# Performance work log

Measured on AMD Instinct MI355X. Metric: run time of the kernel, lower is better.

## Reference

```python
import jax, jax.numpy as jnp
import numpy as np

HEADS = 8
EPS = 1e-4

def pixel_norm(x):
    # faithful to source: mean over dim=1 (token axis for [B,T,C] tensors)
    return x / jnp.sqrt(jnp.mean(x * x, axis=1, keepdims=True) + EPS)

def setup_inputs() -> dict:
    key = jax.random.key(0)
    ks = jax.random.split(key, 6)
    B, T, C = 4, 2048, 512
    s = 1.0 / np.sqrt(C)
    return {
        "hidden_states": jax.random.normal(ks[0], (B, T, C), jnp.float32),
        "Wq": jax.random.normal(ks[1], (C, C), jnp.float32) * s,
        "Wk": jax.random.normal(ks[2], (C, C), jnp.float32) * s,
        "Wv": jax.random.normal(ks[3], (C, C), jnp.float32) * s,
        "Wo": jax.random.normal(ks[4], (C, C), jnp.float32) * s,
        "bo": jnp.zeros((C,), jnp.float32),
    }

def reference(hidden_states, Wq, Wk, Wv, Wo, bo):
    B, T, C = hidden_states.shape
    H = HEADS
    d = C // H
    scale = 1.0 / np.sqrt(d)  # attn.scale = head_dim**-0.5
    residual = hidden_states

    q = pixel_norm(hidden_states @ Wq)  # [B,T,C]
    k = pixel_norm(hidden_states @ Wk)
    v = pixel_norm(hidden_states @ Wv)

    # head_to_batch_dim: [B,T,C] -> [B,H,T,d]
    def split_heads(x):
        return x.reshape(B, T, H, d).transpose(0, 2, 1, 3)
    q, k, v = split_heads(q), split_heads(k), split_heads(v)

    scores = jnp.einsum("bhqd,bhkd->bhqk", q, k) * scale
    probs = jax.nn.softmax(scores, axis=-1)
    out = jnp.einsum("bhqk,bhkd->bhqd", probs, v)  # [B,H,T,d]

    # batch_to_head_dim: [B,H,T,d] -> [B,T,C]
    out = out.transpose(0, 2, 1, 3).reshape(B, T, C)
    out = out @ Wo + bo  # to_out[0]; to_out[1] is dropout (identity in eval)
    out = out + residual  # residual_connection
    return out  # rescale_output_factor = 1.0
```

## Files before the change

kernel.cpp:

```cpp
#include <hip/hip_runtime.h>

#define Tt 2048
#define Cc 512
#define Bb 4
#define BC (Bb * Cc)

typedef __attribute__((ext_vector_type(4))) float f32x4;
typedef __attribute__((ext_vector_type(8))) _Float16 f16x8;
typedef __attribute__((ext_vector_type(4))) _Float16 f16x4;
typedef __attribute__((ext_vector_type(2))) _Float16 f16x2;

__device__ static inline void gl16(const _Float16* g, _Float16* l)
{
    __builtin_amdgcn_global_load_lds(
        (const __attribute__((address_space(1))) void*)g,
        (__attribute__((address_space(3))) void*)l, 16, 0, 0);
}

__global__ __launch_bounds__(256) void wsetup(
    const float* __restrict__ Wq, const float* __restrict__ Wk,
    const float* __restrict__ Wv, const float* __restrict__ Wo,
    _Float16* __restrict__ Wt)
{
    const int z = blockIdx.y;
    const float* W = (z == 0) ? Wq : (z == 1) ? Wk : (z == 2) ? Wv : Wo;
    const int k0 = (blockIdx.x >> 3) * 64, n0 = (blockIdx.x & 7) * 64;
    const int tid = threadIdx.x;
    __shared__ float tile[64][65];

#pragma unroll
    for (int i = 0; i < 4; ++i) {
        const int idx = i * 256 + tid;
        const int kr = idx >> 4, c4 = idx & 15;
        float4 v = *(const float4*)&W[(size_t)(k0 + kr) * Cc + n0 + c4 * 4];
        tile[kr][c4 * 4 + 0] = v.x; tile[kr][c4 * 4 + 1] = v.y;
        tile[kr][c4 * 4 + 2] = v.z; tile[kr][c4 * 4 + 3] = v.w;
    }
    __syncthreads();
#pragma unroll
    for (int i = 0; i < 4; ++i) {
        const int idx = i * 256 + tid;
        const int nr = idx >> 4, k4 = idx & 15;
        f16x4 o;
        o[0] = (_Float16)tile[k4 * 4 + 0][nr];
        o[1] = (_Float16)tile[k4 * 4 + 1][nr];
        o[2] = (_Float16)tile[k4 * 4 + 2][nr];
        o[3] = (_Float16)tile[k4 * 4 + 3][nr];
        *(f16x4*)&Wt[((size_t)(z * 512 + n0 + nr)) * Cc + k0 + k4 * 4] = o;
    }
}

__global__ __launch_bounds__(256) void hs_half(
    const float* __restrict__ HS, _Float16* __restrict__ HSh)
{
    const size_t i = ((size_t)blockIdx.x * 256 + threadIdx.x) * 8;
    float4 a = *(const float4*)&HS[i];
    float4 b = *(const float4*)&HS[i + 4];
    f16x8 o;
    o[0] = (_Float16)a.x; o[1] = (_Float16)a.y;
    o[2] = (_Float16)a.z; o[3] = (_Float16)a.w;
    o[4] = (_Float16)b.x; o[5] = (_Float16)b.y;
    o[6] = (_Float16)b.z; o[7] = (_Float16)b.w;
    *(f16x8*)&HSh[i] = o;
}

__global__ __launch_bounds__(256, 3) void qkv_mfma(
    const _Float16* __restrict__ HSh, const _Float16* __restrict__ Wt,
    _Float16* __restrict__ Qf, _Float16* __restrict__ Kf,
    _Float16* __restrict__ Vf, float* __restrict__ colsum)
{
    const int mt = blockIdx.x;
    const int nt = blockIdx.y;
    const int z  = blockIdx.z;
    _Float16* Out = (z == 0) ? Qf : (z == 1) ? Kf : Vf;

    const int tid = threadIdx.x;
    const int wave = tid >> 6, lane = tid & 63;
    const int quad = lane >> 4, lm = lane & 15;
    const int wm = (wave & 1) * 64, wn = (wave >> 1) * 64;

    __shared__ _Float16 sA[128 * 32];
    __shared__ _Float16 sB[128 * 32];

    f32x4 acc[4][4];
#pragma unroll
    for (int mf = 0; mf < 4; ++mf)
#pragma unroll
        for (int nf = 0; nf < 4; ++nf) acc[mf][nf] = (f32x4){0.f, 0.f, 0.f, 0.f};

    const int lr = lane >> 2;
    const int lc = (lane & 3) * 8;
    const _Float16* gaA = HSh + (size_t)(mt * 128 + wave * 32 + lr) * Cc + lc;
    const _Float16* gaB = Wt + ((size_t)(z * 512 + nt * 128 + wave * 32 + lr)) * Cc + lc;
    _Float16* ldA = &sA[wave * 1024];
    _Float16* ldB = &sB[wave * 1024];

    for (int k0 = 0; k0 < Cc; k0 += 32) {
        __syncthreads();
        gl16(gaA + k0,            ldA);
        gl16(gaA + 16 * Cc + k0,  ldA + 512);
        gl16(gaB + k0,            ldB);
        gl16(gaB + 16 * Cc + k0,  ldB + 512);
        __syncthreads();

        f16x8 ah[4], bh[4];
#pragma unroll
        for (int mf = 0; mf < 4; ++mf)
            ah[mf] = *(const f16x8*)&sA[(wm + mf * 16 + lm) * 32 + quad * 8];
#pragma unroll
        for (int nf = 0; nf < 4; ++nf)
            bh[nf] = *(const f16x8*)&sB[(wn + nf * 16 + lm) * 32 + quad * 8];
#pragma unroll
        for (int mf = 0; mf < 4; ++mf)
#pragma unroll
            for (int nf = 0; nf < 4; ++nf)
                acc[mf][nf] = __builtin_amdgcn_mfma_f32_16x16x32_f16(ah[mf], bh[nf], acc[mf][nf], 0, 0, 0);
    }

    const int bidx = mt >> 4;
#pragma unroll
    for (int nf = 0; nf < 4; ++nf) {
        float cs = 0.f;
#pragma unroll
        for (int mf = 0; mf < 4; ++mf)
#pragma unroll
            for (int r = 0; r < 4; ++r) {
                const float v = acc[mf][nf][r];
                const size_t idx =
                    (size_t)(mt * 128 + wm + mf * 16 + quad * 4 + r) * Cc +
                    nt * 128 + wn + nf * 16 + lm;
                Out[idx] = (_Float16)v;
                cs += v * v;
            }
        cs += __shfl_xor(cs, 16, 64);
        cs += __shfl_xor(cs, 32, 64);
        if (lane < 16)
            atomicAdd(&colsum[(size_t)z * BC + bidx * Cc + nt * 128 + wn + nf * 16 + lane], cs);
    }
}

__global__ void inv_norm_kernel(const float* __restrict__ colsum,
                                float* __restrict__ inv)
{
    const int i = blockIdx.x * blockDim.x + threadIdx.x;
    if (i < 3 * BC) inv[i] = rsqrtf(colsum[i] * (1.0f / Tt) + 1e-4f);
}

__global__ __launch_bounds__(256) void norm_vt(
    const _Float16* __restrict__ V, _Float16* __restrict__ VT)
{
    const int blk = blockIdx.x;
    const int b = blk >> 8, ct = (blk >> 5) & 7, tt = blk & 31;
    const int t0 = tt * 64, c0 = ct * 64;
    const int tid = threadIdx.x;

    __shared__ _Float16 tile[64 * 72];

#pragma unroll
    for (int i = 0; i < 2; ++i) {
        const int idx = i * 256 + tid;
        const int tr = idx >> 3, c8 = (idx & 7) * 8;
        *(f16x8*)&tile[tr * 72 + c8] =
            *(const f16x8*)&V[(size_t)(b * Tt + t0 + tr) * Cc + c0 + c8];
    }
    __syncthreads();
#pragma unroll
    for (int i = 0; i < 2; ++i) {
        const int idx = i * 256 + tid;
        const int cr = idx >> 3, u = idx & 7;
        const int C0 = ((u >> 2) & 1) * 32 + (u & 1) * 16 + ((u >> 1) & 1) * 4;
        f16x4 oa, ob;
#pragma unroll
        for (int j = 0; j < 4; ++j) oa[j] = tile[(u * 8 + j) * 72 + cr];
#pragma unroll
        for (int j = 0; j < 4; ++j) ob[j] = tile[(u * 8 + 4 + j) * 72 + cr];
        _Float16* dst = &VT[(size_t)(b * Cc + c0 + cr) * Tt + t0];
        *(f16x4*)&dst[C0]     = oa;
        *(f16x4*)&dst[C0 + 8] = ob;
    }
}

#define LSTR 72

__global__ __launch_bounds__(256, 3) void attn_mfma(
    const _Float16* __restrict__ Qf, const _Float16* __restrict__ Kf,
    const _Float16* __restrict__ VT, const float* __restrict__ inv,
    _Float16* __restrict__ AO)
{
    const int bid = blockIdx.x;
    const int qt = bid >> 5;
    const int bh = bid & 31;
    const int b = bh >> 3, h = bh & 7;
    const int tid = threadIdx.x;
    const int wave = tid >> 6, lane = tid & 63;
    const int quad = lane >> 4, lm = lane & 15;

    __shared__ _Float16 sK[2][64 * LSTR];
    __shared__ _Float16 sVT[2][64 * LSTR];

    f16x8 qb[2][2];
    {
        const float* iqp = inv + b * Cc + h * 64;
        const float* ikp = inv + BC + b * Cc + h * 64;
#pragma unroll
        for (int qf = 0; qf < 2; ++qf) {
            const int row = qt * 128 + wave * 32 + qf * 16 + lm;
#pragma unroll
            for (int ks = 0; ks < 2; ++ks) {
                const int d0 = ks * 32 + quad * 8;
                f16x8 qv = *(const f16x8*)&Qf[(size_t)(b * Tt + row) * Cc + h * 64 + d0];
#pragma unroll
                for (int j = 0; j < 8; ++j) {
                    const float f = (float)qv[j] * iqp[d0 + j] * ikp[d0 + j] * 0.18033688011f;
                    qb[qf][ks][j] = (_Float16)f;
                }
            }
        }
    }

    f32x4 o[4][2];
#pragma unroll
    for (int cf = 0; cf < 4; ++cf)
#pragma unroll
        for (int qf = 0; qf < 2; ++qf) o[cf][qf] = (f32x4){0.f, 0.f, 0.f, 0.f};
    f32x4 ol[2];
#pragma unroll
    for (int qf = 0; qf < 2; ++qf) ol[qf] = (f32x4){0.f, 0.f, 0.f, 0.f};
    f16x8 ones;
#pragma unroll
    for (int j = 0; j < 8; ++j) ones[j] = (_Float16)1.0f;

    f16x8 pb[2][2];
#pragma unroll
    for (int qf = 0; qf < 2; ++qf)
#pragma unroll
        for (int ks = 0; ks < 2; ++ks)
#pragma unroll
            for (int j = 0; j < 8; ++j) pb[qf][ks][j] = (_Float16)0.0f;

    const int sr0 = tid >> 3, sc0 = (tid & 7) * 8;
    const int sr1 = sr0 + 32;
    const _Float16* gK = Kf + (size_t)b * Tt * Cc + h * 64;
    const _Float16* gV = VT + ((size_t)b * Cc + h * 64) * Tt;

    f16x8 rk0, rk1, rv0, rv1;
    {
        rk0 = *(const f16x8*)&gK[(size_t)sr0 * Cc + sc0];
        rk1 = *(const f16x8*)&gK[(size_t)sr1 * Cc + sc0];
        rv0 = *(const f16x8*)&gV[(size_t)sr0 * Tt + sc0];
        rv1 = *(const f16x8*)&gV[(size_t)sr1 * Tt + sc0];
    }

#pragma unroll 2
    for (int kt = 0; kt < 32; ++kt) {
        const int cur = kt & 1, prv = cur ^ 1;
        _Float16* sKc = sK[cur];
        _Float16* sVc = sVT[cur];

        __syncthreads();
        *(f16x8*)&sKc[sr0 * LSTR + sc0] = rk0;
        *(f16x8*)&sKc[sr1 * LSTR + sc0] = rk1;
        *(f16x8*)&sVc[sr0 * LSTR + sc0] = rv0;
        *(f16x8*)&sVc[sr1 * LSTR + sc0] = rv1;
        __syncthreads();

        if (kt < 31) {
            const int t0 = (kt + 1) * 64;
            rk0 = *(const f16x8*)&gK[(size_t)(t0 + sr0) * Cc + sc0];
            rk1 = *(const f16x8*)&gK[(size_t)(t0 + sr1) * Cc + sc0];
            rv0 = *(const f16x8*)&gV[(size_t)sr0 * Tt + t0 + sc0];
            rv1 = *(const f16x8*)&gV[(size_t)sr1 * Tt + t0 + sc0];
        }

        f32x4 st[4][2];
#pragma unroll
        for (int kf = 0; kf < 4; ++kf)
#pragma unroll
            for (int qf = 0; qf < 2; ++qf) st[kf][qf] = (f32x4){0.f, 0.f, 0.f, 0.f};
#pragma unroll
        for (int ks = 0; ks < 2; ++ks) {
            f16x8 ka[4];
#pragma unroll
            for (int kf = 0; kf < 4; ++kf)
                ka[kf] = *(const f16x8*)&sKc[(kf * 16 + lm) * LSTR + ks * 32 + quad * 8];
            __builtin_amdgcn_s_setprio(1);
#pragma unroll
            for (int kf = 0; kf < 4; ++kf)
#pragma unroll
                for (int qf = 0; qf < 2; ++qf)
                    st[kf][qf] = __builtin_amdgcn_mfma_f32_16x16x32_f16(ka[kf], qb[qf][ks], st[kf][qf], 0, 0, 0);
            __builtin_amdgcn_s_setprio(0);
        }

        if (kt > 0) {
            _Float16* sVp = sVT[prv];
#pragma unroll
            for (int ks = 0; ks < 2; ++ks) {
                f16x8 va[4];
#pragma unroll
                for (int cf = 0; cf < 4; ++cf)
                    va[cf] = *(const f16x8*)&sVp[(cf * 16 + lm) * LSTR + ks * 32 + quad * 8];
                __builtin_amdgcn_s_setprio(1);
#pragma unroll
                for (int cf = 0; cf < 4; ++cf)
#pragma unroll
                    for (int qf = 0; qf < 2; ++qf)
                        o[cf][qf] = __builtin_amdgcn_mfma_f32_16x16x32_f16(va[cf], pb[qf][ks], o[cf][qf], 0, 0, 0);
#pragma unroll
                for (int qf = 0; qf < 2; ++qf)
                    ol[qf] = __builtin_amdgcn_mfma_f32_16x16x32_f16(ones, pb[qf][ks], ol[qf], 0, 0, 0);
                __builtin_amdgcn_s_setprio(0);
            }
        }

#pragma unroll
        for (int ks = 0; ks < 2; ++ks)
#pragma unroll
            for (int qf = 0; qf < 2; ++qf) {
                const f32x4 a = st[2 * ks][qf];
                const f32x4 c = st[2 * ks + 1][qf];
                const f16x2 l0 = __builtin_bit_cast(f16x2, __builtin_amdgcn_cvt_pkrtz(
                    __builtin_amdgcn_exp2f(a[0]), __builtin_amdgcn_exp2f(a[1])));
                const f16x2 l1 = __builtin_bit_cast(f16x2, __builtin_amdgcn_cvt_pkrtz(
                    __builtin_amdgcn_exp2f(a[2]), __builtin_amdgcn_exp2f(a[3])));
                const f16x2 h0 = __builtin_bit_cast(f16x2, __builtin_amdgcn_cvt_pkrtz(
                    __builtin_amdgcn_exp2f(c[0]), __builtin_amdgcn_exp2f(c[1])));
                const f16x2 h1 = __builtin_bit_cast(f16x2, __builtin_amdgcn_cvt_pkrtz(
                    __builtin_amdgcn_exp2f(c[2]), __builtin_amdgcn_exp2f(c[3])));
                f16x8 p;
                p[0] = l0[0]; p[1] = l0[1]; p[2] = l1[0]; p[3] = l1[1];
                p[4] = h0[0]; p[5] = h0[1]; p[6] = h1[0]; p[7] = h1[1];
                pb[qf][ks] = p;
            }
    }

    {
        _Float16* sVp = sVT[1];
#pragma unroll
        for (int ks = 0; ks < 2; ++ks) {
            f16x8 va[4];
#pragma unroll
            for (int cf = 0; cf < 4; ++cf)
                va[cf] = *(const f16x8*)&sVp[(cf * 16 + lm) * LSTR + ks * 32 + quad * 8];
#pragma unroll
            for (int cf = 0; cf < 4; ++cf)
#pragma unroll
                for (int qf = 0; qf < 2; ++qf)
                    o[cf][qf] = __builtin_amdgcn_mfma_f32_16x16x32_f16(va[cf], pb[qf][ks], o[cf][qf], 0, 0, 0);
#pragma unroll
            for (int qf = 0; qf < 2; ++qf)
                ol[qf] = __builtin_amdgcn_mfma_f32_16x16x32_f16(ones, pb[qf][ks], ol[qf], 0, 0, 0);
        }
    }

    float il[2];
#pragma unroll
    for (int qf = 0; qf < 2; ++qf) il[qf] = 1.0f / ol[qf][0];
    const float* ivp = inv + 2 * BC + b * Cc + h * 64;
    float iv[4][4];
#pragma unroll
    for (int cf = 0; cf < 4; ++cf) {
        float4 t = *(const float4*)&ivp[cf * 16 + quad * 4];
        iv[cf][0] = t.x; iv[cf][1] = t.y; iv[cf][2] = t.z; iv[cf][3] = t.w;
    }
#pragma unroll
    for (int qf = 0; qf < 2; ++qf) {
        const size_t row = (size_t)(b * Tt + qt * 128 + wave * 32 + qf * 16 + lm);
#pragma unroll
        for (int cf = 0; cf < 4; ++cf) {
            f16x4 pk;
#pragma unroll
            for (int r = 0; r < 4; ++r)
                pk[r] = (_Float16)(o[cf][qf][r] * il[qf] * iv[cf][r]);
            *(f16x4*)&AO[row * Cc + h * 64 + cf * 16 + quad * 4] = pk;
        }
    }
}

__global__ __launch_bounds__(256, 2) void out_mfma(
    const _Float16* __restrict__ AO, const _Float16* __restrict__ Wt,
    const float* __restrict__ bo, const float* __restrict__ HS,
    float* __restrict__ Outp)
{
    const int mt = blockIdx.x;
    const int nt = blockIdx.y;
    const int tid = threadIdx.x;
    const int wave = tid >> 6, lane = tid & 63;
    const int quad = lane >> 4, lm = lane & 15;
    const int wm = (wave & 1) * 32, wn = (wave >> 1) * 64;

    __shared__ _Float16 sA[64 * 32];
    __shared__ _Float16 sB[128 * 32];

    f32x4 acc[2][4];
#pragma unroll
    for (int mf = 0; mf < 2; ++mf)
#pragma unroll
        for (int nf = 0; nf < 4; ++nf) acc[mf][nf] = (f32x4){0.f, 0.f, 0.f, 0.f};

    const int lr = lane >> 2;
    const int lc = (lane & 3) * 8;
    const _Float16* gaA = AO + (size_t)(mt * 64 + wave * 16 + lr) * Cc + lc;
    const _Float16* gaB = Wt + ((size_t)(3 * 512 + nt * 128 + wave * 32 + lr)) * Cc + lc;
    _Float16* ldA = &sA[wave * 512];
    _Float16* ldB = &sB[wave * 1024];

    for (int k0 = 0; k0 < Cc; k0 += 32) {
        __syncthreads();
        gl16(gaA + k0,           ldA);
        gl16(gaB + k0,           ldB);
        gl16(gaB + 16 * Cc + k0, ldB + 512);
        __syncthreads();

        f16x8 ah[2], bh[4];
#pragma unroll
        for (int mf = 0; mf < 2; ++mf)
            ah[mf] = *(const f16x8*)&sA[(wm + mf * 16 + lm) * 32 + quad * 8];
#pragma unroll
        for (int nf = 0; nf < 4; ++nf)
            bh[nf] = *(const f16x8*)&sB[(wn + nf * 16 + lm) * 32 + quad * 8];
#pragma unroll
        for (int mf = 0; mf < 2; ++mf)
#pragma unroll
            for (int nf = 0; nf < 4; ++nf)
                acc[mf][nf] = __builtin_amdgcn_mfma_f32_16x16x32_f16(ah[mf], bh[nf], acc[mf][nf], 0, 0, 0);
    }

#pragma unroll
    for (int mf = 0; mf < 2; ++mf)
#pragma unroll
        for (int r = 0; r < 4; ++r) {
            const size_t m = (size_t)(mt * 64 + wm + mf * 16 + quad * 4 + r);
#pragma unroll
            for (int nf = 0; nf < 4; ++nf) {
                const int col = nt * 128 + wn + nf * 16 + lm;
                Outp[m * Cc + col] = acc[mf][nf][r] + bo[col] + HS[m * Cc + col];
            }
        }
}

extern "C" void kernel_launch(void* const* d_in, const int* in_sizes, int n_in,
                              void* d_out, int out_size, void* d_ws,
                              size_t ws_size, hipStream_t stream)
{
    const float* HS = (const float*)d_in[0];
    const float* Wq = (const float*)d_in[1];
    const float* Wk = (const float*)d_in[2];
    const float* Wv = (const float*)d_in[3];
    const float* Wo = (const float*)d_in[4];
    const float* bo = (const float*)d_in[5];
    float* out = (float*)d_out;

    const size_t SZ = (size_t)Bb * Tt * Cc;
    _Float16* Qf  = (_Float16*)d_ws;
    _Float16* Kf  = Qf + SZ;
    _Float16* Vf  = Kf + SZ;
    _Float16* VTh = Vf + SZ;
    _Float16* AO  = VTh + SZ;
    _Float16* Wt  = AO + SZ;
    float* colsum = (float*)(Wt + 4 * Cc * Cc);
    float* inv    = colsum + 3 * BC;

    _Float16* HSh = VTh;

    (void)hipMemsetAsync(colsum, 0, 3 * BC * sizeof(float), stream);

    wsetup<<<dim3(64, 4), 256, 0, stream>>>(Wq, Wk, Wv, Wo, Wt);

    hs_half<<<2048, 256, 0, stream>>>(HS, HSh);

    qkv_mfma<<<dim3(64, 4, 3), 256, 0, stream>>>(HSh, Wt, Qf, Kf, Vf, colsum);

    inv_norm_kernel<<<(3 * BC + 255) / 256, 256, 0, stream>>>(colsum, inv);

    norm_vt<<<1024, 256, 0, stream>>>(Vf, VTh);

    attn_mfma<<<dim3(512), 256, 0, stream>>>(Qf, Kf, VTh, inv, AO);

    out_mfma<<<dim3(128, 4), 256, 0, stream>>>(AO, Wt, bo, HS, out);
}
```

Baseline: 163.0 us.

## Merge prep launches and process 128-key blocks per barrier in attention

Weight transpose, hidden-state fp16 cast, and colsum zeroing move into a single prep kernel, and the inverse-norm computation is folded into the norm_vt launch as extra blocks. This removes a memset and two kernel launches. The attention loop now stages two 64-key K/V tiles per barrier pair, which halves the synchronisation count and keeps more loads in flight. In exchange it uses more LDS and registers, so the launch bound drops to 2 blocks per CU.

Measured after the change: 163.5 us. About the same (+0.3%).

```diff
diff --git a/kernel.cpp b/kernel.cpp
--- a/kernel.cpp
+++ b/kernel.cpp
@@ -17,51 +17,56 @@
         (__attribute__((address_space(3))) void*)l, 16, 0, 0);
 }
 
-__global__ __launch_bounds__(256) void wsetup(
+__global__ __launch_bounds__(256) void prep(
     const float* __restrict__ Wq, const float* __restrict__ Wk,
     const float* __restrict__ Wv, const float* __restrict__ Wo,
-    _Float16* __restrict__ Wt)
-{
-    const int z = blockIdx.y;
-    const float* W = (z == 0) ? Wq : (z == 1) ? Wk : (z == 2) ? Wv : Wo;
-    const int k0 = (blockIdx.x >> 3) * 64, n0 = (blockIdx.x & 7) * 64;
+    const float* __restrict__ HS, _Float16* __restrict__ Wt,
+    _Float16* __restrict__ HSh, float* __restrict__ colsum)
+{
+    const int blk = blockIdx.x;
     const int tid = threadIdx.x;
     __shared__ float tile[64][65];
 
-#pragma unroll
-    for (int i = 0; i < 4; ++i) {
-        const int idx = i * 256 + tid;
-        const int kr = idx >> 4, c4 = idx & 15;
-        float4 v = *(const float4*)&W[(size_t)(k0 + kr) * Cc + n0 + c4 * 4];
-        tile[kr][c4 * 4 + 0] = v.x; tile[kr][c4 * 4 + 1] = v.y;
-        tile[kr][c4 * 4 + 2] = v.z; tile[kr][c4 * 4 + 3] = v.w;
-    }
-    __syncthreads();
-#pragma unroll
-    for (int i = 0; i < 4; ++i) {
-        const int idx = i * 256 + tid;
-        const int nr = idx >> 4, k4 = idx & 15;
-        f16x4 o;
-        o[0] = (_Float16)tile[k4 * 4 + 0][nr];
-        o[1] = (_Float16)tile[k4 * 4 + 1][nr];
-        o[2] = (_Float16)tile[k4 * 4 + 2][nr];
-        o[3] = (_Float16)tile[k4 * 4 + 3][nr];
-        *(f16x4*)&Wt[((size_t)(z * 512 + n0 + nr)) * Cc + k0 + k4 * 4] = o;
-    }
-}
-
-__global__ __launch_bounds__(256) void hs_half(
-    const float* __restrict__ HS, _Float16* __restrict__ HSh)
-{
-    const size_t i = ((size_t)blockIdx.x * 256 + threadIdx.x) * 8;
-    float4 a = *(const float4*)&HS[i];
-    float4 b = *(const float4*)&HS[i + 4];
-    f16x8 o;
-    o[0] = (_Float16)a.x; o[1] = (_Float16)a.y;
-    o[2] = (_Float16)a.z; o[3] = (_Float16)a.w;
-    o[4] = (_Float16)b.x; o[5] = (_Float16)b.y;
-    o[6] = (_Float16)b.z; o[7] = (_Float16)b.w;
-    *(f16x8*)&HSh[i] = o;
+    if (blk < 2048) {
+        const size_t i = ((size_t)blk * 256 + tid) * 8;
+        float4 a = *(const float4*)&HS[i];
+        float4 b = *(const float4*)&HS[i + 4];
+        f16x8 o;
+        o[0] = (_Float16)a.x; o[1] = (_Float16)a.y;
+        o[2] = (_Float16)a.z; o[3] = (_Float16)a.w;
+        o[4] = (_Float16)b.x; o[5] = (_Float16)b.y;
+        o[6] = (_Float16)b.z; o[7] = (_Float16)b.w;
+        *(f16x8*)&HSh[i] = o;
+    } else if (blk < 2304) {
+        const int lb = blk - 2048;
+        const int z = lb >> 6, x = lb & 63;
+        const float* W = (z == 0) ? Wq : (z == 1) ? Wk : (z == 2) ? Wv : Wo;
+        const int k0 = (x >> 3) * 64, n0 = (x & 7) * 64;
+#pragma unroll
+        for (int i = 0; i < 4; ++i) {
+            const int idx = i * 256 + tid;
+            const int kr = idx >> 4, c4 = idx & 15;
+            float4 v = *(const float4*)&W[(size_t)(k0 + kr) * Cc + n0 + c4 * 4];
+            tile[kr][c4 * 4 + 0] = v.x; tile[kr][c4 * 4 + 1] = v.y;
+            tile[kr][c4 * 4 + 2] = v.z; tile[kr][c4 * 4 + 3] = v.w;
+        }
+        __syncthreads();
+#pragma unroll
+        for (int i = 0; i < 4; ++i) {
+            const int idx = i * 256 + tid;
+            const int nr = idx >> 4, k4 = idx & 15;
+            f16x4 o;
+            o[0] = (_Float16)tile[k4 * 4 + 0][nr];
+            o[1] = (_Float16)tile[k4 * 4 + 1][nr];
+            o[2] = (_Float16)tile[k4 * 4 + 2][nr];
+            o[3] = (_Float16)tile[k4 * 4 + 3][nr];
+            *(f16x4*)&Wt[((size_t)(z * 512 + n0 + nr)) * Cc + k0 + k4 * 4] = o;
+        }
+    } else {
+        const int i = (blk - 2304) * 2048 + tid * 8;
+        *(f32x4*)&colsum[i]     = (f32x4){0.f, 0.f, 0.f, 0.f};
+        *(f32x4*)&colsum[i + 4] = (f32x4){0.f, 0.f, 0.f, 0.f};
+    }
 }
 
 __global__ __launch_bounds__(256, 3) void qkv_mfma(
@@ -139,22 +144,23 @@
     }
 }
 
-__global__ void inv_norm_kernel(const float* __restrict__ colsum,
-                                float* __restrict__ inv)
-{
-    const int i = blockIdx.x * blockDim.x + threadIdx.x;
-    if (i < 3 * BC) inv[i] = rsqrtf(colsum[i] * (1.0f / Tt) + 1e-4f);
-}
-
 __global__ __launch_bounds__(256) void norm_vt(
-    const _Float16* __restrict__ V, _Float16* __restrict__ VT)
+    const _Float16* __restrict__ V, _Float16* __restrict__ VT,
+    const float* __restrict__ colsum, float* __restrict__ inv)
 {
     const int blk = blockIdx.x;
+    const int tid = threadIdx.x;
+
+    __shared__ _Float16 tile[64 * 72];
+
+    if (blk >= 1024) {
+        const int i = (blk - 1024) * 256 + tid;
+        inv[i] = rsqrtf(colsum[i] * (1.0f / Tt) + 1e-4f);
+        return;
+    }
+
     const int b = blk >> 8, ct = (blk >> 5) & 7, tt = blk & 31;
     const int t0 = tt * 64, c0 = ct * 64;
-    const int tid = threadIdx.x;
-
-    __shared__ _Float16 tile[64 * 72];
 
 #pragma unroll
     for (int i = 0; i < 2; ++i) {
@@ -182,7 +188,7 @@
 
 #define LSTR 72
 
-__global__ __launch_bounds__(256, 3) void attn_mfma(
+__global__ __launch_bounds__(256, 2) void attn_mfma(
     const _Float16* __restrict__ Qf, const _Float16* __restrict__ Kf,
     const _Float16* __restrict__ VT, const float* __restrict__ inv,
     _Float16* __restrict__ AO)
@@ -196,7 +202,7 @@
     const int quad = lane >> 4, lm = lane & 15;
 
     __shared__ _Float16 sK[2][64 * LSTR];
-    __shared__ _Float16 sVT[2][64 * LSTR];
+    __shared__ _Float16 sVT[2][2][64 * LSTR];
 
     f16x8 qb[2][2];
     {
@@ -243,99 +249,113 @@
     const _Float16* gK = Kf + (size_t)b * Tt * Cc + h * 64;
     const _Float16* gV = VT + ((size_t)b * Cc + h * 64) * Tt;
 
-    f16x8 rk0, rk1, rv0, rv1;
+    f16x8 rka0, rka1, rva0, rva1;
+    f16x8 rkb0, rkb1, rvb0, rvb1;
     {
-        rk0 = *(const f16x8*)&gK[(size_t)sr0 * Cc + sc0];
-        rk1 = *(const f16x8*)&gK[(size_t)sr1 * Cc + sc0];
-        rv0 = *(const f16x8*)&gV[(size_t)sr0 * Tt + sc0];
-        rv1 = *(const f16x8*)&gV[(size_t)sr1 * Tt + sc0];
+        rka0 = *(const f16x8*)&gK[(size_t)sr0 * Cc + sc0];
+        rka1 = *(const f16x8*)&gK[(size_t)sr1 * Cc + sc0];
+        rva0 = *(const f16x8*)&gV[(size_t)sr0 * Tt + sc0];
+        rva1 = *(const f16x8*)&gV[(size_t)sr1 * Tt + sc0];
+        rkb0 = *(const f16x8*)&gK[(size_t)(64 + sr0) * Cc + sc0];
+        rkb1 = *(const f16x8*)&gK[(size_t)(64 + sr1) * Cc + sc0];
+        rvb0 = *(const f16x8*)&gV[(size_t)sr0 * Tt + 64 + sc0];
+        rvb1 = *(const f16x8*)&gV[(size_t)sr1 * Tt + 64 + sc0];
     }
 
 #pragma unroll 2
-    for (int kt = 0; kt < 32; ++kt) {
-        const int cur = kt & 1, prv = cur ^ 1;
-        _Float16* sKc = sK[cur];
-        _Float16* sVc = sVT[cur];
-
-        __syncthreads();
-        *(f16x8*)&sKc[sr0 * LSTR + sc0] = rk0;
-        *(f16x8*)&sKc[sr1 * LSTR + sc0] = rk1;
-        *(f16x8*)&sVc[sr0 * LSTR + sc0] = rv0;
-        *(f16x8*)&sVc[sr1 * LSTR + sc0] = rv1;
-        __syncthreads();
-
-        if (kt < 31) {
-            const int t0 = (kt + 1) * 64;
-            rk0 = *(const f16x8*)&gK[(size_t)(t0 + sr0) * Cc + sc0];
-            rk1 = *(const f16x8*)&gK[(size_t)(t0 + sr1) * Cc + sc0];
-            rv0 = *(const f16x8*)&gV[(size_t)sr0 * Tt + t0 + sc0];
-            rv1 = *(const f16x8*)&gV[(size_t)sr1 * Tt + t0 + sc0];
-        }
-
-        f32x4 st[4][2];
-#pragma unroll
-        for (int kf = 0; kf < 4; ++kf)
-#pragma unroll
-            for (int qf = 0; qf < 2; ++qf) st[kf][qf] = (f32x4){0.f, 0.f, 0.f, 0.f};
-#pragma unroll
-        for (int ks = 0; ks < 2; ++ks) {
-            f16x8 ka[4];
+    for (int r = 0; r < 16; ++r) {
+        const int g = r & 1;
+
+        __syncthreads();
+        *(f16x8*)&sK[0][sr0 * LSTR + sc0] = rka0;
+        *(f16x8*)&sK[0][sr1 * LSTR + sc0] = rka1;
+        *(f16x8*)&sVT[g][0][sr0 * LSTR + sc0] = rva0;
+        *(f16x8*)&sVT[g][0][sr1 * LSTR + sc0] = rva1;
+        *(f16x8*)&sK[1][sr0 * LSTR + sc0] = rkb0;
+        *(f16x8*)&sK[1][sr1 * LSTR + sc0] = rkb1;
+        *(f16x8*)&sVT[g][1][sr0 * LSTR + sc0] = rvb0;
+        *(f16x8*)&sVT[g][1][sr1 * LSTR + sc0] = rvb1;
+        __syncthreads();
+
+        if (r < 15) {
+            const int tn = (r + 1) * 128;
+            rka0 = *(const f16x8*)&gK[(size_t)(tn + sr0) * Cc + sc0];
+            rka1 = *(const f16x8*)&gK[(size_t)(tn + sr1) * Cc + sc0];
+            rva0 = *(const f16x8*)&gV[(size_t)sr0 * Tt + tn + sc0];
+            rva1 = *(const f16x8*)&gV[(size_t)sr1 * Tt + tn + sc0];
+            rkb0 = *(const f16x8*)&gK[(size_t)(tn + 64 + sr0) * Cc + sc0];
+            rkb1 = *(const f16x8*)&gK[(size_t)(tn + 64 + sr1) * Cc + sc0];
+            rvb0 = *(const f16x8*)&gV[(size_t)sr0 * Tt + tn + 64 + sc0];
+            rvb1 = *(const f16x8*)&gV[(size_t)sr1 * Tt + tn + 64 + sc0];
+        }
+
+#pragma unroll
+        for (int half = 0; half < 2; ++half) {
+            f32x4 st[4][2];
 #pragma unroll
             for (int kf = 0; kf < 4; ++kf)
-                ka[kf] = *(const f16x8*)&sKc[(kf * 16 + lm) * LSTR + ks * 32 + quad * 8];
-            __builtin_amdgcn_s_setprio(1);
-#pragma unroll
-            for (int kf = 0; kf < 4; ++kf)
-#pragma unroll
-                for (int qf = 0; qf < 2; ++qf)
-                    st[kf][qf] = __builtin_amdgcn_mfma_f32_16x16x32_f16(ka[kf], qb[qf][ks], st[kf][qf], 0, 0, 0);
-            __builtin_amdgcn_s_setprio(0);
-        }
-
-        if (kt > 0) {
-            _Float16* sVp = sVT[prv];
+#pragma unroll
+                for (int qf = 0; qf < 2; ++qf) st[kf][qf] = (f32x4){0.f, 0.f, 0.f, 0.f};
 #pragma unroll
             for (int ks = 0; ks < 2; ++ks) {
-                f16x8 va[4];
-#pragma unroll
-                for (int cf = 0; cf < 4; ++cf)
-                    va[cf] = *(const f16x8*)&sVp[(cf * 16 + lm) * LSTR + ks * 32 + quad * 8];
+                f16x8 ka[4];
+#pragma unroll
+                for (int kf = 0; kf < 4; ++kf)
+                    ka[kf] = *(const f16x8*)&sK[half][(kf * 16 + lm) * LSTR + ks * 32 + quad * 8];
                 __builtin_amdgcn_s_setprio(1);
 #pragma unroll
-                for (int cf = 0; cf < 4; ++cf)
+                for (int kf = 0; kf < 4; ++kf)
 #pragma unroll
                     for (int qf = 0; qf < 2; ++qf)
-                        o[cf][qf] = __builtin_amdgcn_mfma_f32_16x16x32_f16(va[cf], pb[qf][ks], o[cf][qf], 0, 0, 0);
-#pragma unroll
-                for (int qf = 0; qf < 2; ++qf)
-                    ol[qf] = __builtin_amdgcn_mfma_f32_16x16x32_f16(ones, pb[qf][ks], ol[qf], 0, 0, 0);
+                        st[kf][qf] = __builtin_amdgcn_mfma_f32_16x16x32_f16(ka[kf], qb[qf][ks], st[kf][qf], 0, 0, 0);
                 __builtin_amdgcn_s_setprio(0);
             }
-        }
-
-#pragma unroll
-        for (int ks = 0; ks < 2; ++ks)
-#pragma unroll
-            for (int qf = 0; qf < 2; ++qf) {
-                const f32x4 a = st[2 * ks][qf];
-                const f32x4 c = st[2 * ks + 1][qf];
-                const f16x2 l0 = __builtin_bit_cast(f16x2, __builtin_amdgcn_cvt_pkrtz(
-                    __builtin_amdgcn_exp2f(a[0]), __builtin_amdgcn_exp2f(a[1])));
-                const f16x2 l1 = __builtin_bit_cast(f16x2, __builtin_amdgcn_cvt_pkrtz(
-                    __builtin_amdgcn_exp2f(a[2]), __builtin_amdgcn_exp2f(a[3])));
-                const f16x2 h0 = __builtin_bit_cast(f16x2, __builtin_amdgcn_cvt_pkrtz(
-                    __builtin_amdgcn_exp2f(c[0]), __builtin_amdgcn_exp2f(c[1])));
-                const f16x2 h1 = __builtin_bit_cast(f16x2, __builtin_amdgcn_cvt_pkrtz(
-                    __builtin_amdgcn_exp2f(c[2]), __builtin_amdgcn_exp2f(c[3])));
-                f16x8 p;
-                p[0] = l0[0]; p[1] = l0[1]; p[2] = l1[0]; p[3] = l1[1];
-                p[4] = h0[0]; p[5] = h0[1]; p[6] = h1[0]; p[7] = h1[1];
-                pb[qf][ks] = p;
+
+            if (half == 1 || r > 0) {
+                const _Float16* sVp = (half == 0) ? sVT[g ^ 1][1] : sVT[g][0];
+#pragma unroll
+                for (int ks = 0; ks < 2; ++ks) {
+                    f16x8 va[4];
+#pragma unroll
+                    for (int cf = 0; cf < 4; ++cf)
+                        va[cf] = *(const f16x8*)&sVp[(cf * 16 + lm) * LSTR + ks * 32 + quad * 8];
+                    __builtin_amdgcn_s_setprio(1);
+#pragma unroll
+                    for (int cf = 0; cf < 4; ++cf)
+#pragma unroll
+                        for (int qf = 0; qf < 2; ++qf)
+                            o[cf][qf] = __builtin_amdgcn_mfma_f32_16x16x32_f16(va[cf], pb[qf][ks], o[cf][qf], 0, 0, 0);
+#pragma unroll
+                    for (int qf = 0; qf < 2; ++qf)
+                        ol[qf] = __builtin_amdgcn_mfma_f32_16x16x32_f16(ones, pb[qf][ks], ol[qf], 0, 0, 0);
+                    __builtin_amdgcn_s_setprio(0);
+                }
             }
+
+#pragma unroll
+            for (int ks = 0; ks < 2; ++ks)
+#pragma unroll
+                for (int qf = 0; qf < 2; ++qf) {
+                    const f32x4 a = st[2 * ks][qf];
+                    const f32x4 c = st[2 * ks + 1][qf];
+                    const f16x2 l0 = __builtin_bit_cast(f16x2, __builtin_amdgcn_cvt_pkrtz(
+                        __builtin_amdgcn_exp2f(a[0]), __builtin_amdgcn_exp2f(a[1])));
+                    const f16x2 l1 = __builtin_bit_cast(f16x2, __builtin_amdgcn_cvt_pkrtz(
+                        __builtin_amdgcn_exp2f(a[2]), __builtin_amdgcn_exp2f(a[3])));
+                    const f16x2 h0 = __builtin_bit_cast(f16x2, __builtin_amdgcn_cvt_pkrtz(
+                        __builtin_amdgcn_exp2f(c[0]), __builtin_amdgcn_exp2f(c[1])));
+                    const f16x2 h1 = __builtin_bit_cast(f16x2, __builtin_amdgcn_cvt_pkrtz(
+                        __builtin_amdgcn_exp2f(c[2]), __builtin_amdgcn_exp2f(c[3])));
+                    f16x8 p;
+                    p[0] = l0[0]; p[1] = l0[1]; p[2] = l1[0]; p[3] = l1[1];
+                    p[4] = h0[0]; p[5] = h0[1]; p[6] = h1[0]; p[7] = h1[1];
+                    pb[qf][ks] = p;
+                }
+        }
     }
 
     {
-        _Float16* sVp = sVT[1];
+        const _Float16* sVp = sVT[1][1];
 #pragma unroll
         for (int ks = 0; ks < 2; ++ks) {
             f16x8 va[4];
@@ -463,17 +483,11 @@
 
     _Float16* HSh = VTh;
 
-    (void)hipMemsetAsync(colsum, 0, 3 * BC * sizeof(float), stream);
-
-    wsetup<<<dim3(64, 4), 256, 0, stream>>>(Wq, Wk, Wv, Wo, Wt);
-
-    hs_half<<<2048, 256, 0, stream>>>(HS, HSh);
+    prep<<<2307, 256, 0, stream>>>(Wq, Wk, Wv, Wo, HS, Wt, HSh, colsum);
 
     qkv_mfma<<<dim3(64, 4, 3), 256, 0, stream>>>(HSh, Wt, Qf, Kf, Vf, colsum);
 
-    inv_norm_kernel<<<(3 * BC + 255) / 256, 256, 0, stream>>>(colsum, inv);
-
-    norm_vt<<<1024, 256, 0, stream>>>(Vf, VTh);
+    norm_vt<<<1048, 256, 0, stream>>>(Vf, VTh, colsum, inv);
 
     attn_mfma<<<dim3(512), 256, 0, stream>>>(Qf, Kf, VTh, inv, AO);
 
```

## Fuse prep kernels, write V transposed from QKV GEMM, inline inverse norms

Applied to the files above, without the earlier changes.

Merges the weight transpose, hidden-state half conversion and colsum zeroing into one prep launch, which replaces a memset and two kernels. The V projection now writes its transposed, permuted layout straight from the GEMM epilogue through a larger shared-memory staging buffer, which removes the separate norm_vt pass and its extra round trip of V. Inverse norms are computed inside the attention kernel from the colsums, so inv_norm_kernel is gone. This cuts launch count and memory traffic. In exchange, the QKV kernel's shared memory grows and the attention kernel does some redundant rsqrt work.

Result: faster. 154.0 us (median of 3 runs) (-5.5%).

```diff
diff --git a/kernel.cpp b/kernel.cpp
--- a/kernel.cpp
+++ b/kernel.cpp
@@ -17,70 +17,75 @@
         (__attribute__((address_space(3))) void*)l, 16, 0, 0);
 }
 
-__global__ __launch_bounds__(256) void wsetup(
+__global__ __launch_bounds__(256) void prep(
     const float* __restrict__ Wq, const float* __restrict__ Wk,
     const float* __restrict__ Wv, const float* __restrict__ Wo,
-    _Float16* __restrict__ Wt)
-{
-    const int z = blockIdx.y;
-    const float* W = (z == 0) ? Wq : (z == 1) ? Wk : (z == 2) ? Wv : Wo;
-    const int k0 = (blockIdx.x >> 3) * 64, n0 = (blockIdx.x & 7) * 64;
+    const float* __restrict__ HS, _Float16* __restrict__ Wt,
+    _Float16* __restrict__ HSh, float* __restrict__ colsum)
+{
+    const int blk = blockIdx.x;
     const int tid = threadIdx.x;
     __shared__ float tile[64][65];
 
-#pragma unroll
-    for (int i = 0; i < 4; ++i) {
-        const int idx = i * 256 + tid;
-        const int kr = idx >> 4, c4 = idx & 15;
-        float4 v = *(const float4*)&W[(size_t)(k0 + kr) * Cc + n0 + c4 * 4];
-        tile[kr][c4 * 4 + 0] = v.x; tile[kr][c4 * 4 + 1] = v.y;
-        tile[kr][c4 * 4 + 2] = v.z; tile[kr][c4 * 4 + 3] = v.w;
-    }
-    __syncthreads();
-#pragma unroll
-    for (int i = 0; i < 4; ++i) {
-        const int idx = i * 256 + tid;
-        const int nr = idx >> 4, k4 = idx & 15;
-        f16x4 o;
-        o[0] = (_Float16)tile[k4 * 4 + 0][nr];
-        o[1] = (_Float16)tile[k4 * 4 + 1][nr];
-        o[2] = (_Float16)tile[k4 * 4 + 2][nr];
-        o[3] = (_Float16)tile[k4 * 4 + 3][nr];
-        *(f16x4*)&Wt[((size_t)(z * 512 + n0 + nr)) * Cc + k0 + k4 * 4] = o;
-    }
-}
-
-__global__ __launch_bounds__(256) void hs_half(
-    const float* __restrict__ HS, _Float16* __restrict__ HSh)
-{
-    const size_t i = ((size_t)blockIdx.x * 256 + threadIdx.x) * 8;
-    float4 a = *(const float4*)&HS[i];
-    float4 b = *(const float4*)&HS[i + 4];
-    f16x8 o;
-    o[0] = (_Float16)a.x; o[1] = (_Float16)a.y;
-    o[2] = (_Float16)a.z; o[3] = (_Float16)a.w;
-    o[4] = (_Float16)b.x; o[5] = (_Float16)b.y;
-    o[6] = (_Float16)b.z; o[7] = (_Float16)b.w;
-    *(f16x8*)&HSh[i] = o;
+    if (blk < 2048) {
+        const size_t i = ((size_t)blk * 256 + tid) * 8;
+        float4 a = *(const float4*)&HS[i];
+        float4 b = *(const float4*)&HS[i + 4];
+        f16x8 o;
+        o[0] = (_Float16)a.x; o[1] = (_Float16)a.y;
+        o[2] = (_Float16)a.z; o[3] = (_Float16)a.w;
+        o[4] = (_Float16)b.x; o[5] = (_Float16)b.y;
+        o[6] = (_Float16)b.z; o[7] = (_Float16)b.w;
+        *(f16x8*)&HSh[i] = o;
+    } else if (blk < 2304) {
+        const int lb = blk - 2048;
+        const int z = lb >> 6, x = lb & 63;
+        const float* W = (z == 0) ? Wq : (z == 1) ? Wk : (z == 2) ? Wv : Wo;
+        const int k0 = (x >> 3) * 64, n0 = (x & 7) * 64;
+#pragma unroll
+        for (int i = 0; i < 4; ++i) {
+            const int idx = i * 256 + tid;
+            const int kr = idx >> 4, c4 = idx & 15;
+            float4 v = *(const float4*)&W[(size_t)(k0 + kr) * Cc + n0 + c4 * 4];
+            tile[kr][c4 * 4 + 0] = v.x; tile[kr][c4 * 4 + 1] = v.y;
+            tile[kr][c4 * 4 + 2] = v.z; tile[kr][c4 * 4 + 3] = v.w;
+        }
+        __syncthreads();
+#pragma unroll
+        for (int i = 0; i < 4; ++i) {
+            const int idx = i * 256 + tid;
+            const int nr = idx >> 4, k4 = idx & 15;
+            f16x4 o;
+            o[0] = (_Float16)tile[k4 * 4 + 0][nr];
+            o[1] = (_Float16)tile[k4 * 4 + 1][nr];
+            o[2] = (_Float16)tile[k4 * 4 + 2][nr];
+            o[3] = (_Float16)tile[k4 * 4 + 3][nr];
+            *(f16x4*)&Wt[((size_t)(z * 512 + n0 + nr)) * Cc + k0 + k4 * 4] = o;
+        }
+    } else {
+        const int i = (blk - 2304) * 2048 + tid * 8;
+        *(f32x4*)&colsum[i]     = (f32x4){0.f, 0.f, 0.f, 0.f};
+        *(f32x4*)&colsum[i + 4] = (f32x4){0.f, 0.f, 0.f, 0.f};
+    }
 }
 
 __global__ __launch_bounds__(256, 3) void qkv_mfma(
     const _Float16* __restrict__ HSh, const _Float16* __restrict__ Wt,
     _Float16* __restrict__ Qf, _Float16* __restrict__ Kf,
-    _Float16* __restrict__ Vf, float* __restrict__ colsum)
+    _Float16* __restrict__ VTh, float* __restrict__ colsum)
 {
     const int mt = blockIdx.x;
     const int nt = blockIdx.y;
     const int z  = blockIdx.z;
-    _Float16* Out = (z == 0) ? Qf : (z == 1) ? Kf : Vf;
 
     const int tid = threadIdx.x;
     const int wave = tid >> 6, lane = tid & 63;
     const int quad = lane >> 4, lm = lane & 15;
     const int wm = (wave & 1) * 64, wn = (wave >> 1) * 64;
 
-    __shared__ _Float16 sA[128 * 32];
-    __shared__ _Float16 sB[128 * 32];
+    __shared__ _Float16 smem[128 * 136];
+    _Float16* sA = smem;
+    _Float16* sB = smem + 128 * 32;
 
     f32x4 acc[4][4];
 #pragma unroll
@@ -118,6 +123,8 @@
     }
 
     const int bidx = mt >> 4;
+
+    _Float16* Out = (z == 0) ? Qf : Kf;
 #pragma unroll
     for (int nf = 0; nf < 4; ++nf) {
         float cs = 0.f;
@@ -126,57 +133,49 @@
 #pragma unroll
             for (int r = 0; r < 4; ++r) {
                 const float v = acc[mf][nf][r];
-                const size_t idx =
-                    (size_t)(mt * 128 + wm + mf * 16 + quad * 4 + r) * Cc +
-                    nt * 128 + wn + nf * 16 + lm;
-                Out[idx] = (_Float16)v;
                 cs += v * v;
+                if (z < 2) {
+                    const size_t idx =
+                        (size_t)(mt * 128 + wm + mf * 16 + quad * 4 + r) * Cc +
+                        nt * 128 + wn + nf * 16 + lm;
+                    Out[idx] = (_Float16)v;
+                }
             }
         cs += __shfl_xor(cs, 16, 64);
         cs += __shfl_xor(cs, 32, 64);
         if (lane < 16)
             atomicAdd(&colsum[(size_t)z * BC + bidx * Cc + nt * 128 + wn + nf * 16 + lane], cs);
     }
-}
-
-__global__ void inv_norm_kernel(const float* __restrict__ colsum,
-                                float* __restrict__ inv)
-{
-    const int i = blockIdx.x * blockDim.x + threadIdx.x;
-    if (i < 3 * BC) inv[i] = rsqrtf(colsum[i] * (1.0f / Tt) + 1e-4f);
-}
-
-__global__ __launch_bounds__(256) void norm_vt(
-    const _Float16* __restrict__ V, _Float16* __restrict__ VT)
-{
-    const int blk = blockIdx.x;
-    const int b = blk >> 8, ct = (blk >> 5) & 7, tt = blk & 31;
-    const int t0 = tt * 64, c0 = ct * 64;
-    const int tid = threadIdx.x;
-
-    __shared__ _Float16 tile[64 * 72];
-
-#pragma unroll
-    for (int i = 0; i < 2; ++i) {
-        const int idx = i * 256 + tid;
-        const int tr = idx >> 3, c8 = (idx & 7) * 8;
-        *(f16x8*)&tile[tr * 72 + c8] =
-            *(const f16x8*)&V[(size_t)(b * Tt + t0 + tr) * Cc + c0 + c8];
-    }
-    __syncthreads();
-#pragma unroll
-    for (int i = 0; i < 2; ++i) {
-        const int idx = i * 256 + tid;
-        const int cr = idx >> 3, u = idx & 7;
-        const int C0 = ((u >> 2) & 1) * 32 + (u & 1) * 16 + ((u >> 1) & 1) * 4;
-        f16x4 oa, ob;
-#pragma unroll
-        for (int j = 0; j < 4; ++j) oa[j] = tile[(u * 8 + j) * 72 + cr];
-#pragma unroll
-        for (int j = 0; j < 4; ++j) ob[j] = tile[(u * 8 + 4 + j) * 72 + cr];
-        _Float16* dst = &VT[(size_t)(b * Cc + c0 + cr) * Tt + t0];
-        *(f16x4*)&dst[C0]     = oa;
-        *(f16x4*)&dst[C0 + 8] = ob;
+
+    if (z == 2) {
+        __syncthreads();
+#pragma unroll
+        for (int nf = 0; nf < 4; ++nf) {
+            const int c = wn + nf * 16 + lm;
+#pragma unroll
+            for (int mf = 0; mf < 4; ++mf) {
+                const int m0 = wm + mf * 16 + quad * 4;
+                const int tl = m0 & 63;
+                const int u = tl >> 3, j0 = tl & 7;
+                const int p0 = ((u >> 2) & 1) * 32 + (u & 1) * 16 +
+                               ((u >> 1) & 1) * 4 + ((j0 >= 4) ? 8 : 0);
+                const int tperm = (m0 & 64) + p0;
+                f16x4 pk;
+#pragma unroll
+                for (int r = 0; r < 4; ++r) pk[r] = (_Float16)acc[mf][nf][r];
+                *(f16x4*)&smem[c * 136 + tperm] = pk;
+            }
+        }
+        __syncthreads();
+        const int b = mt >> 4;
+        const int tbase = (mt & 15) * 128;
+#pragma unroll
+        for (int i = 0; i < 8; ++i) {
+            const int idx = i * 256 + tid;
+            const int cr = idx >> 4, t8 = (idx & 15) * 8;
+            f16x8 v = *(const f16x8*)&smem[cr * 136 + t8];
+            *(f16x8*)&VTh[((size_t)(b * Cc) + nt * 128 + cr) * Tt + tbase + t8] = v;
+        }
     }
 }
 
@@ -184,7 +183,7 @@
 
 __global__ __launch_bounds__(256, 3) void attn_mfma(
     const _Float16* __restrict__ Qf, const _Float16* __restrict__ Kf,
-    const _Float16* __restrict__ VT, const float* __restrict__ inv,
+    const _Float16* __restrict__ VT, const float* __restrict__ colsum,
     _Float16* __restrict__ AO)
 {
     const int bid = blockIdx.x;
@@ -194,14 +193,29 @@
     const int tid = threadIdx.x;
     const int wave = tid >> 6, lane = tid & 63;
     const int quad = lane >> 4, lm = lane & 15;
+    const float invT = 1.0f / Tt;
 
     __shared__ _Float16 sK[2][64 * LSTR];
     __shared__ _Float16 sVT[2][64 * LSTR];
 
+    float ss[2][8];
+    {
+        const float* csq = colsum + b * Cc + h * 64;
+        const float* csk = colsum + BC + b * Cc + h * 64;
+#pragma unroll
+        for (int ks = 0; ks < 2; ++ks) {
+            const int d0 = ks * 32 + quad * 8;
+#pragma unroll
+            for (int j = 0; j < 8; ++j) {
+                const float iq = rsqrtf(csq[d0 + j] * invT + 1e-4f);
+                const float ik = rsqrtf(csk[d0 + j] * invT + 1e-4f);
+                ss[ks][j] = iq * ik * 0.18033688011f;
+            }
+        }
+    }
+
     f16x8 qb[2][2];
     {
-        const float* iqp = inv + b * Cc + h * 64;
-        const float* ikp = inv + BC + b * Cc + h * 64;
 #pragma unroll
         for (int qf = 0; qf < 2; ++qf) {
             const int row = qt * 128 + wave * 32 + qf * 16 + lm;
@@ -210,10 +224,8 @@
                 const int d0 = ks * 32 + quad * 8;
                 f16x8 qv = *(const f16x8*)&Qf[(size_t)(b * Tt + row) * Cc + h * 64 + d0];
 #pragma unroll
-                for (int j = 0; j < 8; ++j) {
-                    const float f = (float)qv[j] * iqp[d0 + j] * ikp[d0 + j] * 0.18033688011f;
-                    qb[qf][ks][j] = (_Float16)f;
-                }
+                for (int j = 0; j < 8; ++j)
+                    qb[qf][ks][j] = (_Float16)((float)qv[j] * ss[ks][j]);
             }
         }
     }
@@ -356,12 +368,15 @@
     float il[2];
 #pragma unroll
     for (int qf = 0; qf < 2; ++qf) il[qf] = 1.0f / ol[qf][0];
-    const float* ivp = inv + 2 * BC + b * Cc + h * 64;
+    const float* csv = colsum + 2 * BC + b * Cc + h * 64;
     float iv[4][4];
 #pragma unroll
     for (int cf = 0; cf < 4; ++cf) {
-        float4 t = *(const float4*)&ivp[cf * 16 + quad * 4];
-        iv[cf][0] = t.x; iv[cf][1] = t.y; iv[cf][2] = t.z; iv[cf][3] = t.w;
+        float4 t = *(const float4*)&csv[cf * 16 + quad * 4];
+        iv[cf][0] = rsqrtf(t.x * invT + 1e-4f);
+        iv[cf][1] = rsqrtf(t.y * invT + 1e-4f);
+        iv[cf][2] = rsqrtf(t.z * invT + 1e-4f);
+        iv[cf][3] = rsqrtf(t.w * invT + 1e-4f);
     }
 #pragma unroll
     for (int qf = 0; qf < 2; ++qf) {
@@ -454,28 +469,17 @@
     const size_t SZ = (size_t)Bb * Tt * Cc;
     _Float16* Qf  = (_Float16*)d_ws;
     _Float16* Kf  = Qf + SZ;
-    _Float16* Vf  = Kf + SZ;
-    _Float16* VTh = Vf + SZ;
-    _Float16* AO  = VTh + SZ;
+    _Float16* VTh = Kf + SZ;
+    _Float16* HSh = VTh + SZ;
+    _Float16* AO  = HSh + SZ;
     _Float16* Wt  = AO + SZ;
     float* colsum = (float*)(Wt + 4 * Cc * Cc);
-    float* inv    = colsum + 3 * BC;
-
-    _Float16* HSh = VTh;
-
-    (void)hipMemsetAsync(colsum, 0, 3 * BC * sizeof(float), stream);
-
-    wsetup<<<dim3(64, 4), 256, 0, stream>>>(Wq, Wk, Wv, Wo, Wt);
-
-    hs_half<<<2048, 256, 0, stream>>>(HS, HSh);
-
-    qkv_mfma<<<dim3(64, 4, 3), 256, 0, stream>>>(HSh, Wt, Qf, Kf, Vf, colsum);
-
-    inv_norm_kernel<<<(3 * BC + 255) / 256, 256, 0, stream>>>(colsum, inv);
-
-    norm_vt<<<1024, 256, 0, stream>>>(Vf, VTh);
-
-    attn_mfma<<<dim3(512), 256, 0, stream>>>(Qf, Kf, VTh, inv, AO);
+
+    prep<<<2307, 256, 0, stream>>>(Wq, Wk, Wv, Wo, HS, Wt, HSh, colsum);
+
+    qkv_mfma<<<dim3(64, 4, 3), 256, 0, stream>>>(HSh, Wt, Qf, Kf, VTh, colsum);
+
+    attn_mfma<<<dim3(512), 256, 0, stream>>>(Qf, Kf, VTh, colsum, AO);
 
     out_mfma<<<dim3(128, 4), 256, 0, stream>>>(AO, Wt, bo, HS, out);
 }
```
